# Optimization experiments

Hardware: AMD Instinct MI355X
Metric: run time of the kernel (lower is better)

Reference implementation:

```python
import jax, jax.numpy as jnp
import numpy as np

N_NODES = 100000
N_EDGES = 1600000
D_IN = 128
D_HID = 128
D_OUT = 16
N_LAYERS = 3
N_GRAPHS = 64
EPS = 1e-12


def _glorot(key, shape):
    fan_in = shape[-1]
    bound = 1.0 / np.sqrt(fan_in)
    return jax.random.uniform(key, shape, jnp.float32, -bound, bound)


def setup_inputs() -> dict:
    key = jax.random.key(0)
    ks = jax.random.split(key, 12)
    x = jax.random.normal(ks[0], (N_NODES, D_IN), jnp.float32)
    edge_index = jax.random.randint(ks[1], (2, N_EDGES), 0, N_NODES, jnp.int64)
    batch = jnp.sort(jax.random.randint(ks[2], (N_NODES,), 0, N_GRAPHS, jnp.int64))
    # stacked GraphSage weights: torch Linear stores [out, in]
    Wl = _glorot(ks[3], (N_LAYERS, D_HID, D_IN))
    bl = _glorot(ks[4], (N_LAYERS, D_HID))
    Wr = _glorot(ks[5], (N_LAYERS, D_HID, D_IN))
    br = _glorot(ks[6], (N_LAYERS, D_HID))
    W1 = _glorot(ks[7], (D_HID, D_HID))
    b1 = _glorot(ks[8], (D_HID,))
    W2 = _glorot(ks[9], (D_OUT, D_HID))
    b2 = _glorot(ks[10], (D_OUT,))
    return {"x": x, "edge_index": edge_index, "batch": batch,
            "Wl": Wl, "bl": bl, "Wr": Wr, "br": br,
            "W1": W1, "b1": b1, "W2": W2, "b2": b2}


def reference(x, edge_index, batch, Wl, bl, Wr, br, W1, b1, W2, b2):
    N = x.shape[0]
    src, dst = edge_index[0], edge_index[1]
    # in-degree for mean aggregation (clamped to avoid div-by-zero)
    deg = jax.ops.segment_sum(jnp.ones_like(dst, dtype=x.dtype), dst, num_segments=N)
    deg = jnp.maximum(deg, 1.0)[:, None]
    h = x
    for i in range(N_LAYERS):
        # lin_r applied at nodes, then gathered (equivalent to lin_r(x_j) per edge)
        hr = h @ Wr[i].T + br[i]
        msg = hr[src]                               # [E, D_HID] gather
        agg = jax.ops.segment_sum(msg, dst, num_segments=N) / deg  # scatter-mean
        out = agg + (h @ Wl[i].T + bl[i])
        # F.normalize(out) -> L2 norm along dim=1, eps=1e-12
        nrm = jnp.maximum(jnp.linalg.norm(out, axis=1, keepdims=True), EPS)
        h = jax.nn.relu(out / nrm)                  # dropout is identity (eval)
    # post message-passing MLP (dropout identity in eval mode)
    h = h @ W1.T + b1
    h = h @ W2.T + b2
    # global mean pool over graphs
    cnt = jnp.maximum(jax.ops.segment_sum(jnp.ones_like(batch, dtype=h.dtype), batch, num_segments=N_GRAPHS), 1.0)
    pooled = jax.ops.segment_sum(h, batch, num_segments=N_GRAPHS) / cnt[:, None]
    return jax.nn.log_softmax(pooled, axis=1)
```

## Files before the change

### kernel.cpp

```cpp
#include <hip/hip_runtime.h>
#include <cstdint>
#include <cstddef>

#define NN 100000
#define NE 1600000
#define DD 128
#define NG 64
#define NB 782
#define GB 1563

#if defined(__has_builtin)
#if __has_builtin(__builtin_amdgcn_cvt_pk_f32_fp8) && __has_builtin(__builtin_amdgcn_cvt_pk_fp8_f32)
#define USE_FP8 1
#endif
#endif
#ifndef USE_FP8
#define USE_FP8 0
#endif

using bf16x8 = __attribute__((ext_vector_type(8))) short;
using f32x4  = __attribute__((ext_vector_type(4))) float;
using f32x2  = __attribute__((ext_vector_type(2))) float;

__device__ __forceinline__ int clampi(int v, int hi) {
    v = v < 0 ? 0 : v;
    return v >= hi ? hi - 1 : v;
}
__device__ __forceinline__ unsigned short f2bf(float f) {
    unsigned int u = __float_as_uint(f);
    u += 0x7fffu + ((u >> 16) & 1u);
    return (unsigned short)(u >> 16);
}
__device__ __forceinline__ float bf2f(unsigned short s) {
    return __uint_as_float(((unsigned int)s) << 16);
}
#if USE_FP8
__device__ __forceinline__ unsigned char f2fp8(float v) {
    return (unsigned char)(__builtin_amdgcn_cvt_pk_fp8_f32(v, 0.f, 0, false) & 0xFF);
}
__device__ __forceinline__ void acc_row(f32x2* a2, uint2 v) {
    f32x2 p;
    p = __builtin_amdgcn_cvt_pk_f32_fp8(v.x, false); a2[0] += p;
    p = __builtin_amdgcn_cvt_pk_f32_fp8(v.x, true);  a2[1] += p;
    p = __builtin_amdgcn_cvt_pk_f32_fp8(v.y, false); a2[2] += p;
    p = __builtin_amdgcn_cvt_pk_f32_fp8(v.y, true);  a2[3] += p;
}
#endif

#define WTOT (3 * 256 * 128)
__global__ void cvtw_kernel(const float* __restrict__ Wl, const float* __restrict__ Wr,
                            unsigned short* __restrict__ Wcat3,
                            int* __restrict__ bcnt, int* __restrict__ gcur0,
                            float* __restrict__ pooled, float* __restrict__ cnt) {
    int t = blockIdx.x * 256 + threadIdx.x;
    if (t < NB) { bcnt[t] = 0; gcur0[t] = 0; }
    if (t < NG * DD) pooled[t] = 0.f;
    if (t < NG) cnt[t] = 0.f;
    if (t < WTOT) {
        int j    = t & 7;
        int lane = (t >> 3) & 63;
        int ks   = (t >> 9) & 3;
        int n    = (t >> 11) & 7;
        int half = (t >> 14) & 1;
        int l    = t >> 15;
        int l15 = lane & 15, lg = lane >> 4;
        int o = n * 16 + l15;
        int k = ks * 32 + lg * 8 + j;
        const float* Wsrc = half ? Wr : Wl;
        Wcat3[t] = f2bf(Wsrc[(size_t)l * 16384 + o * 128 + k]);
    }
}

template <bool F32IN>
__global__ __launch_bounds__(256) void gemm4_kernel(
    const void* __restrict__ hin_, const unsigned short* __restrict__ Wf,
    const float* __restrict__ bl, unsigned short* __restrict__ zb,
    unsigned char* __restrict__ ub, const int* __restrict__ dst,
    int* __restrict__ bcnt, int nG) {
    __shared__ unsigned short lA[64 * 128];
    __shared__ unsigned short sstz[64][136];

    if (blockIdx.x >= nG) {
        int* lcnt = (int*)lA;
        for (int i = threadIdx.x; i < NB; i += 256) lcnt[i] = 0;
        __syncthreads();
        int b = blockIdx.x - nG;
        int e0 = b * 8000;
        int e1 = e0 + 8000; if (e1 > NE) e1 = NE;
        for (int e = e0 + threadIdx.x; e < e1; e += 256)
            atomicAdd(&lcnt[clampi(dst[e], NN) >> 7], 1);
        __syncthreads();
        for (int i = threadIdx.x; i < NB; i += 256)
            if (lcnt[i]) atomicAdd(&bcnt[i], lcnt[i]);
        return;
    }

    const int tid = threadIdx.x;
    const int w = tid >> 6, l = tid & 63;
    const int l15 = l & 15, lg = l >> 4;
    const int n0 = blockIdx.x * 64;

#pragma unroll
    for (int q = 0; q < 4; ++q) {
        int d = (q * 256 + tid) * 16;
        int row = d >> 8;
        int colb = d & 255;
        int srow = n0 + row; srow = srow < NN ? srow : NN - 1;
        bf16x8 v;
        if (F32IN) {
            const float* rp = (const float*)hin_ + (size_t)srow * DD + (colb >> 1);
            const float4 f0 = *(const float4*)rp;
            const float4 f1 = *(const float4*)(rp + 4);
            v[0] = (short)f2bf(f0.x); v[1] = (short)f2bf(f0.y);
            v[2] = (short)f2bf(f0.z); v[3] = (short)f2bf(f0.w);
            v[4] = (short)f2bf(f1.x); v[5] = (short)f2bf(f1.y);
            v[6] = (short)f2bf(f1.z); v[7] = (short)f2bf(f1.w);
        } else {
            v = *(const bf16x8*)((const unsigned short*)hin_ + (size_t)srow * DD + (colb >> 1));
        }
        int sd = d ^ (((d >> 8) & 7) << 4);
        *(bf16x8*)((char*)lA + sd) = v;
    }
    __syncthreads();

    const int half = w >> 1, rt = w & 1;

    bf16x8 a[4][2];
#pragma unroll
    for (int ks = 0; ks < 4; ++ks)
#pragma unroll
        for (int m = 0; m < 2; ++m) {
            int row = rt * 32 + m * 16 + l15;
            int L = row * 256 + ks * 64 + lg * 16;
            int SL = L ^ (((L >> 8) & 7) << 4);
            a[ks][m] = *(const bf16x8*)((char*)lA + SL);
        }

    f32x4 acc[2][8];
#pragma unroll
    for (int m = 0; m < 2; ++m)
#pragma unroll
        for (int n = 0; n < 8; ++n) acc[m][n] = (f32x4){0.f, 0.f, 0.f, 0.f};

    const unsigned short* Wb = Wf + ((size_t)half << 14);
#pragma unroll
    for (int ks = 0; ks < 4; ++ks) {
#pragma unroll
        for (int n = 0; n < 8; ++n) {
            bf16x8 b = *(const bf16x8*)(Wb + (((n << 2) + ks) << 9) + (l << 3));
            acc[0][n] = __builtin_amdgcn_mfma_f32_16x16x32_bf16(a[ks][0], b, acc[0][n], 0, 0, 0);
            acc[1][n] = __builtin_amdgcn_mfma_f32_16x16x32_bf16(a[ks][1], b, acc[1][n], 0, 0, 0);
        }
    }

    __syncthreads();

    if (half == 0) {
        float blv[8];
#pragma unroll
        for (int n = 0; n < 8; ++n) blv[n] = bl[n * 16 + l15];
#pragma unroll
        for (int m = 0; m < 2; ++m)
#pragma unroll
            for (int r = 0; r < 4; ++r) {
                int brow = rt * 32 + m * 16 + lg * 4 + r;
#pragma unroll
                for (int n = 0; n < 8; ++n)
                    sstz[brow][n * 16 + l15] = f2bf(acc[m][n][r] + blv[n]);
            }
#pragma unroll
        for (int p = 0; p < 8; ++p) {
            int brow = rt * 32 + p * 4 + lg;
            int node = n0 + brow;
            bf16x8 vv = *(const bf16x8*)(&sstz[brow][l15 * 8]);
            if (node < NN)
                *(bf16x8*)(zb + (size_t)node * DD + l15 * 8) = vv;
        }
    } else {
#if USE_FP8
        unsigned char* sstu = (unsigned char*)lA;
#pragma unroll
        for (int m = 0; m < 2; ++m)
#pragma unroll
            for (int r = 0; r < 4; ++r) {
                int brow = rt * 32 + m * 16 + lg * 4 + r;
#pragma unroll
                for (int n = 0; n < 8; ++n)
                    sstu[brow * 136 + n * 16 + l15] = f2fp8(acc[m][n][r]);
            }
        __builtin_amdgcn_s_waitcnt(0);
#pragma unroll
        for (int p = 0; p < 8; ++p) {
            int brow = rt * 32 + p * 4 + lg;
            int node = n0 + brow;
            uint2 vv = *(const uint2*)(sstu + brow * 136 + l15 * 8);
            if (node < NN)
                *(uint2*)(ub + (size_t)node * DD + l15 * 8) = vv;
        }
#else
        unsigned short* ub16 = (unsigned short*)ub;
#pragma unroll
        for (int m = 0; m < 2; ++m)
#pragma unroll
            for (int r = 0; r < 4; ++r) {
                int brow = rt * 32 + m * 16 + lg * 4 + r;
                int node = n0 + brow;
                if (node < NN)
#pragma unroll
                    for (int n = 0; n < 8; ++n)
                        ub16[(size_t)node * DD + n * 16 + l15] = f2bf(acc[m][n][r]);
            }
#endif
    }
}

__global__ __launch_bounds__(256) void bpart2_kernel(
    const int* __restrict__ src, const int* __restrict__ dst,
    const int* __restrict__ bcnt, int* __restrict__ gcur0,
    int* __restrict__ bstart_g, unsigned* __restrict__ stage) {
    __shared__ int bst[NB];
    __shared__ int lcnt[NB];
    __shared__ int partial[256];
    const int t = threadIdx.x;
    int own[4]; int ssum = 0;
#pragma unroll
    for (int q = 0; q < 4; ++q) {
        int idx = t * 4 + q;
        own[q] = (idx < NB) ? bcnt[idx] : 0;
        ssum += own[q];
    }
    partial[t] = ssum;
    __syncthreads();
    for (int d = 1; d < 256; d <<= 1) {
        int v = (t >= d) ? partial[t - d] : 0;
        __syncthreads();
        partial[t] += v;
        __syncthreads();
    }
    int run = partial[t] - ssum;
#pragma unroll
    for (int q = 0; q < 4; ++q) {
        int idx = t * 4 + q;
        if (idx < NB) bst[idx] = run;
        run += own[q];
    }
    if (blockIdx.x == 0) {
#pragma unroll
        for (int q = 0; q < 4; ++q) {
            int idx = t * 4 + q;
            if (idx < NB) bstart_g[idx] = bst[idx];
        }
        if (t == 0) bstart_g[NB] = NE;
    }
    for (int i = t; i < NB; i += 256) lcnt[i] = 0;
    __syncthreads();
    int e0 = blockIdx.x * 8000;
    int e1 = e0 + 8000; if (e1 > NE) e1 = NE;
    for (int e = e0 + t; e < e1; e += 256)
        atomicAdd(&lcnt[clampi(dst[e], NN) >> 7], 1);
    __syncthreads();
    for (int i = t; i < NB; i += 256) {
        int c = lcnt[i];
        if (c) lcnt[i] = bst[i] + atomicAdd(&gcur0[i], c);
    }
    __syncthreads();
    for (int e = e0 + t; e < e1; e += 256) {
        int d = clampi(dst[e], NN);
        int pos = atomicAdd(&lcnt[d >> 7], 1);
        stage[pos] = (unsigned)clampi(src[e], NN) | ((unsigned)(d & 127) << 17);
    }
}

__global__ __launch_bounds__(256) void bfill_kernel(
    const unsigned* __restrict__ stage, const int* __restrict__ bstart,
    int* __restrict__ row_ptr, int* __restrict__ csr) {
    __shared__ int scnt[128];
    __shared__ int scur[128];
    const int b = blockIdx.x;
    const int t = threadIdx.x;
    const int s0 = bstart[b], s1 = bstart[b + 1];
    const int n0 = b << 7;
    int nend = NN - n0; if (nend > 128) nend = 128;
    if (t < 128) scnt[t] = 0;
    __syncthreads();
    for (int i = s0 + t; i < s1; i += 256)
        atomicAdd(&scnt[stage[i] >> 17], 1);
    __syncthreads();
    int own = (t < 128) ? scnt[t] : 0;
    for (int d = 1; d < 128; d <<= 1) {
        int v = (t < 128 && t >= d) ? scnt[t - d] : 0;
        __syncthreads();
        if (t < 128) scnt[t] += v;
        __syncthreads();
    }
    if (t < 128) {
        int excl = scnt[t] - own;
        scur[t] = excl;
        if (t < nend) row_ptr[n0 + t] = s0 + excl;
    }
    if (b == NB - 1 && t == 0) row_ptr[NN] = NE;
    __syncthreads();
    for (int i = s0 + t; i < s1; i += 256) {
        unsigned p = stage[i];
        int slot = atomicAdd(&scur[p >> 17], 1);
        csr[s0 + slot] = (int)(p & 0x1FFFFu);
    }
}

__global__ __launch_bounds__(256) void pullc4_kernel(
    const unsigned char* __restrict__ u, const unsigned short* __restrict__ z,
    const float* __restrict__ br, const int* __restrict__ row_ptr,
    const int* __restrict__ csr, unsigned short* __restrict__ hOut) {
    int w = threadIdx.x >> 6, lane = threadIdx.x & 63;
    int n = blockIdx.x * 4 + w;
    if (n >= NN) return;
    int g = lane >> 4, c = lane & 15;
    int s0 = row_ptr[n], s1 = row_ptr[n + 1];
    int len = s1 - s0;
    float inv = 1.0f / (float)(len > 0 ? len : 1);
    int idxv = (s0 + lane < s1) ? csr[s0 + lane] : 0;
    bf16x8 zv = *(const bf16x8*)(z + (size_t)n * DD + c * 8);
#if USE_FP8
    f32x2 a2[4];
#pragma unroll
    for (int q = 0; q < 4; ++q) a2[q] = (f32x2){0.f, 0.f};
    int lcap = len < 64 ? len : 64;
    int r = g;
    for (; r + 12 < lcap; r += 16) {
        int i0 = __shfl(idxv, r);
        int i1 = __shfl(idxv, r + 4);
        int i2 = __shfl(idxv, r + 8);
        int i3 = __shfl(idxv, r + 12);
        uint2 v0 = *(const uint2*)(u + (size_t)i0 * DD + c * 8);
        uint2 v1 = *(const uint2*)(u + (size_t)i1 * DD + c * 8);
        uint2 v2 = *(const uint2*)(u + (size_t)i2 * DD + c * 8);
        uint2 v3 = *(const uint2*)(u + (size_t)i3 * DD + c * 8);
        acc_row(a2, v0); acc_row(a2, v1); acc_row(a2, v2); acc_row(a2, v3);
    }
    for (; r < lcap; r += 4) {
        int i0 = __shfl(idxv, r);
        uint2 v0 = *(const uint2*)(u + (size_t)i0 * DD + c * 8);
        acc_row(a2, v0);
    }
    for (int j = s0 + 64 + g; j < s1; j += 4) {
        uint2 v0 = *(const uint2*)(u + (size_t)csr[j] * DD + c * 8);
        acc_row(a2, v0);
    }
    float acc[8];
#pragma unroll
    for (int q = 0; q < 4; ++q) { acc[q * 2] = a2[q].x; acc[q * 2 + 1] = a2[q].y; }
#else
    const unsigned short* ub16 = (const unsigned short*)u;
    float acc[8];
#pragma unroll
    for (int q = 0; q < 8; ++q) acc[q] = 0.f;
    int lcap = len < 64 ? len : 64;
    int r = g;
    for (; r < lcap; r += 4) {
        int i0 = __shfl(idxv, r);
        bf16x8 v0 = *(const bf16x8*)(ub16 + (size_t)i0 * DD + c * 8);
#pragma unroll
        for (int q = 0; q < 8; ++q) acc[q] += bf2f((unsigned short)v0[q]);
    }
    for (int j = s0 + 64 + g; j < s1; j += 4) {
        bf16x8 v0 = *(const bf16x8*)(ub16 + (size_t)csr[j] * DD + c * 8);
#pragma unroll
        for (int q = 0; q < 8; ++q) acc[q] += bf2f((unsigned short)v0[q]);
    }
#endif
#pragma unroll
    for (int q = 0; q < 8; ++q) {
        acc[q] += __shfl_xor(acc[q], 16);
        acc[q] += __shfl_xor(acc[q], 32);
    }
    const float4 br0 = *(const float4*)(br + c * 8);
    const float4 br1 = *(const float4*)(br + c * 8 + 4);
    float bg = len > 0 ? 1.f : 0.f;
    float v[8]; float ss = 0.f;
#pragma unroll
    for (int q = 0; q < 8; ++q) {
        float brq = (q < 4) ? (&br0.x)[q] : (&br1.x)[q - 4];
        v[q] = acc[q] * inv + bf2f((unsigned short)zv[q]) + bg * brq;
        ss = fmaf(v[q], v[q], ss);
    }
    ss += __shfl_xor(ss, 1); ss += __shfl_xor(ss, 2);
    ss += __shfl_xor(ss, 4); ss += __shfl_xor(ss, 8);
    float invn = 1.0f / fmaxf(sqrtf(ss), 1e-12f);
    if (g == 0) {
        bf16x8 rr;
#pragma unroll
        for (int q = 0; q < 8; ++q) rr[q] = (short)f2bf(fmaxf(v[q], 0.f) * invn);
        *(bf16x8*)(hOut + (size_t)n * DD + c * 8) = rr;
    }
}

__global__ __launch_bounds__(256) void pool_bf16(
    const unsigned short* __restrict__ h, const int* __restrict__ batch,
    float* __restrict__ pooled, float* __restrict__ cnt) {
    int hw = (blockIdx.x * blockDim.x + threadIdx.x) >> 5;
    int lane = threadIdx.x & 31;
    int total_hw = (gridDim.x * blockDim.x) >> 5;
    int chunk = (NN + total_hw - 1) / total_hw;
    int nbeg = hw * chunk;
    int nend = nbeg + chunk; if (nend > NN) nend = NN;
    if (nbeg >= nend) return;
    float ax = 0.f, ay = 0.f, az = 0.f, aw = 0.f;
    int curg = clampi(batch[nbeg], NG);
    int run = 0;
    for (int n = nbeg; n < nend; ++n) {
        int g = clampi(batch[n], NG);
        if (g != curg) {
            atomicAdd(&pooled[curg * DD + lane * 4 + 0], ax);
            atomicAdd(&pooled[curg * DD + lane * 4 + 1], ay);
            atomicAdd(&pooled[curg * DD + lane * 4 + 2], az);
            atomicAdd(&pooled[curg * DD + lane * 4 + 3], aw);
            if (lane == 0) atomicAdd(&cnt[curg], (float)run);
            ax = ay = az = aw = 0.f; run = 0; curg = g;
        }
        const ushort4 v = *(const ushort4*)(h + (size_t)n * DD + lane * 4);
        ax += bf2f(v.x); ay += bf2f(v.y); az += bf2f(v.z); aw += bf2f(v.w);
        ++run;
    }
    atomicAdd(&pooled[curg * DD + lane * 4 + 0], ax);
    atomicAdd(&pooled[curg * DD + lane * 4 + 1], ay);
    atomicAdd(&pooled[curg * DD + lane * 4 + 2], az);
    atomicAdd(&pooled[curg * DD + lane * 4 + 3], aw);
    if (lane == 0) atomicAdd(&cnt[curg], (float)run);
}

__global__ __launch_bounds__(1024) void tail_kernel(
    const float* __restrict__ pooled, const float* __restrict__ cnt,
    const float* __restrict__ W1, const float* __restrict__ b1,
    const float* __restrict__ W2, const float* __restrict__ b2,
    float* __restrict__ out) {
    __shared__ float Wc[16][128];
    __shared__ float bcs[16];
    int t = threadIdx.x;
    for (int i = t; i < 2048; i += 1024) {
        int o = i >> 7, k = i & 127;
        float s = 0.f;
        for (int j = 0; j < 128; ++j) s = fmaf(W2[o * 128 + j], W1[j * 128 + k], s);
        Wc[o][k] = s;
    }
    if (t < 16) {
        float sb = 0.f;
        for (int j = 0; j < 128; ++j) sb = fmaf(W2[t * 128 + j], b1[j], sb);
        bcs[t] = sb + b2[t];
    }
    __syncthreads();
    int g = t >> 4, o = t & 15;
    float invc = 1.0f / fmaxf(cnt[g], 1.0f);
    float z = bcs[o];
    for (int k = 0; k < 128; ++k) z = fmaf(pooled[g * DD + k] * invc, Wc[o][k], z);
    float m = z;
    m = fmaxf(m, __shfl_xor(m, 1)); m = fmaxf(m, __shfl_xor(m, 2));
    m = fmaxf(m, __shfl_xor(m, 4)); m = fmaxf(m, __shfl_xor(m, 8));
    float e = expf(z - m);
    float s = e;
    s += __shfl_xor(s, 1); s += __shfl_xor(s, 2);
    s += __shfl_xor(s, 4); s += __shfl_xor(s, 8);
    out[g * 16 + o] = z - m - logf(s);
}

__global__ void zero_out_kernel(float* __restrict__ out, int n) {
    int i = blockIdx.x * 256 + threadIdx.x;
    if (i < n) out[i] = 0.f;
}

extern "C" void kernel_launch(void* const* d_in, const int* in_sizes, int n_in,
                              void* d_out, int out_size, void* d_ws, size_t ws_size,
                              hipStream_t stream) {
    const float* x  = (const float*)d_in[0];
    const int*   ei = (const int*)d_in[1];
    const int* batch = (const int*)d_in[2];
    const float* Wl = (const float*)d_in[3];
    const float* bl = (const float*)d_in[4];
    const float* Wr = (const float*)d_in[5];
    const float* br = (const float*)d_in[6];
    const float* W1 = (const float*)d_in[7];
    const float* b1 = (const float*)d_in[8];
    const float* W2 = (const float*)d_in[9];
    const float* b2 = (const float*)d_in[10];
    float* out = (float*)d_out;

    const int* src = ei;
    const int* dst = ei + NE;

    char* ws = (char*)d_ws;
    size_t off = 0;
    auto alloc = [&](size_t bytes) -> void* {
        void* p = ws + off; off += (bytes + 255) & ~(size_t)255; return p;
    };
    unsigned short* hA    = (unsigned short*)alloc((size_t)NN * DD * 2);
    unsigned short* hB    = (unsigned short*)alloc((size_t)NN * DD * 2);
    unsigned short* zb    = (unsigned short*)alloc((size_t)NN * DD * 2);
    unsigned char*  ub    = (unsigned char*)alloc((size_t)NN * DD * 2);
    unsigned short* Wcat3 = (unsigned short*)alloc((size_t)WTOT * 2);
    int* row_ptr  = (int*)alloc((size_t)(NN + 1) * 4);
    int* csr      = (int*)alloc((size_t)NE * 4);
    unsigned* stage = (unsigned*)alloc((size_t)NE * 4);
    int* bcnt     = (int*)alloc((size_t)NB * 4);
    int* bstart   = (int*)alloc((size_t)(NB + 1) * 4);
    int* gcur0    = (int*)alloc((size_t)NB * 4);
    float* pooled = (float*)alloc(NG * DD * 4);
    float* cnt    = (float*)alloc(NG * 4);

    if (off > ws_size) {
        zero_out_kernel<<<(out_size + 255) / 256, 256, 0, stream>>>(out, out_size);
        return;
    }

    cvtw_kernel<<<(WTOT + 255) / 256, 256, 0, stream>>>(
        Wl, Wr, Wcat3, bcnt, gcur0, pooled, cnt);

    const int npb = (NE + 7999) / 8000;

    gemm4_kernel<true><<<GB + npb, 256, 0, stream>>>(
        x, Wcat3, bl, zb, ub, dst, bcnt, GB);

    bpart2_kernel<<<npb, 256, 0, stream>>>(src, dst, bcnt, gcur0, bstart, stage);
    bfill_kernel<<<NB, 256, 0, stream>>>(stage, bstart, row_ptr, csr);

    unsigned short* bufs[2] = {hA, hB};
    pullc4_kernel<<<(NN + 3) / 4, 256, 0, stream>>>(
        ub, zb, br, row_ptr, csr, bufs[0]);
    const unsigned short* hin = bufs[0];
    for (int l = 1; l < 3; ++l) {
        gemm4_kernel<false><<<GB, 256, 0, stream>>>(
            hin, Wcat3 + (size_t)l * 32768, bl + (size_t)l * 128,
            zb, ub, dst, bcnt, GB);
        pullc4_kernel<<<(NN + 3) / 4, 256, 0, stream>>>(
            ub, zb, br + (size_t)l * 128, row_ptr, csr, bufs[l & 1]);
        hin = bufs[l & 1];
    }

    pool_bf16<<<256, 256, 0, stream>>>(hin, batch, pooled, cnt);
    tail_kernel<<<1, 1024, 0, stream>>>(pooled, cnt, W1, b1, W2, b2, out);
}
```

Measured before the change: 350.1 us.

## Reshuffle CSR build stages and widen GEMM blocks to 512 threads

Moves the bucket-counting histogram into the weight-conversion kernel and folds the bucket partition (prefix scan plus staging scatter) into the first GEMM launch as extra blocks, so the separate bpart2 kernel disappears. The bcnt/gcur0 zeroing becomes a hipMemsetAsync over adjacent buffers. The GEMM switches to 512 threads with 8 waves, each computing a 16-row tile instead of 32, which halves per-wave accumulators and may raise occupancy. This removes one launch and overlaps partitioning with GEMM work, at the cost of a larger block and an extra memset call.

```diff
diff --git a/kernel.cpp b/kernel.cpp
--- a/kernel.cpp
+++ b/kernel.cpp
@@ -48,12 +48,27 @@
 #endif
 
 #define WTOT (3 * 256 * 128)
-__global__ void cvtw_kernel(const float* __restrict__ Wl, const float* __restrict__ Wr,
-                            unsigned short* __restrict__ Wcat3,
-                            int* __restrict__ bcnt, int* __restrict__ gcur0,
-                            float* __restrict__ pooled, float* __restrict__ cnt) {
+#define CVB 384
+__global__ __launch_bounds__(256) void cvth_kernel(
+    const float* __restrict__ Wl, const float* __restrict__ Wr,
+    unsigned short* __restrict__ Wcat3,
+    float* __restrict__ pooled, float* __restrict__ cnt,
+    const int* __restrict__ dst, int* __restrict__ bcnt) {
+    __shared__ int lcnt[NB];
+    if (blockIdx.x >= CVB) {
+        for (int i = threadIdx.x; i < NB; i += 256) lcnt[i] = 0;
+        __syncthreads();
+        int b = blockIdx.x - CVB;
+        int e0 = b * 8000;
+        int e1 = e0 + 8000; if (e1 > NE) e1 = NE;
+        for (int e = e0 + threadIdx.x; e < e1; e += 256)
+            atomicAdd(&lcnt[clampi(dst[e], NN) >> 7], 1);
+        __syncthreads();
+        for (int i = threadIdx.x; i < NB; i += 256)
+            if (lcnt[i]) atomicAdd(&bcnt[i], lcnt[i]);
+        return;
+    }
     int t = blockIdx.x * 256 + threadIdx.x;
-    if (t < NB) { bcnt[t] = 0; gcur0[t] = 0; }
     if (t < NG * DD) pooled[t] = 0.f;
     if (t < NG) cnt[t] = 0.f;
     if (t < WTOT) {
@@ -72,26 +87,69 @@
 }
 
 template <bool F32IN>
-__global__ __launch_bounds__(256) void gemm4_kernel(
+__global__ __launch_bounds__(512) void gemm5_kernel(
     const void* __restrict__ hin_, const unsigned short* __restrict__ Wf,
     const float* __restrict__ bl, unsigned short* __restrict__ zb,
-    unsigned char* __restrict__ ub, const int* __restrict__ dst,
-    int* __restrict__ bcnt, int nG) {
+    unsigned char* __restrict__ ub,
+    const int* __restrict__ src, const int* __restrict__ dst,
+    const int* __restrict__ bcnt, int* __restrict__ gcur0,
+    int* __restrict__ bstart_g, unsigned* __restrict__ stage, int nG) {
     __shared__ unsigned short lA[64 * 128];
     __shared__ unsigned short sstz[64][136];
 
     if (blockIdx.x >= nG) {
-        int* lcnt = (int*)lA;
-        for (int i = threadIdx.x; i < NB; i += 256) lcnt[i] = 0;
+        int* bst  = (int*)lA;
+        int* lcnt = (int*)(lA + 2048);
+        int* partial = (int*)(&sstz[0][0]);
+        const int t = threadIdx.x;
+        int own[2]; int ssum = 0;
+#pragma unroll
+        for (int q = 0; q < 2; ++q) {
+            int idx = t * 2 + q;
+            own[q] = (idx < NB) ? bcnt[idx] : 0;
+            ssum += own[q];
+        }
+        partial[t] = ssum;
+        __syncthreads();
+        for (int d = 1; d < 512; d <<= 1) {
+            int v = (t >= d) ? partial[t - d] : 0;
+            __syncthreads();
+            partial[t] += v;
+            __syncthreads();
+        }
+        int run = partial[t] - ssum;
+#pragma unroll
+        for (int q = 0; q < 2; ++q) {
+            int idx = t * 2 + q;
+            if (idx < NB) bst[idx] = run;
+            run += own[q];
+        }
+        if (blockIdx.x == nG) {
+#pragma unroll
+            for (int q = 0; q < 2; ++q) {
+                int idx = t * 2 + q;
+                if (idx < NB) bstart_g[idx] = bst[idx];
+            }
+            if (t == 0) bstart_g[NB] = NE;
+        }
+        for (int i = t; i < NB; i += 512) lcnt[i] = 0;
         __syncthreads();
         int b = blockIdx.x - nG;
         int e0 = b * 8000;
         int e1 = e0 + 8000; if (e1 > NE) e1 = NE;
-        for (int e = e0 + threadIdx.x; e < e1; e += 256)
+        for (int e = e0 + t; e < e1; e += 512)
             atomicAdd(&lcnt[clampi(dst[e], NN) >> 7], 1);
         __syncthreads();
-        for (int i = threadIdx.x; i < NB; i += 256)
-            if (lcnt[i]) atomicAdd(&bcnt[i], lcnt[i]);
+        for (int i = t; i < NB; i += 512) {
+            int c = lcnt[i];
+            if (c) lcnt[i] = bst[i] + atomicAdd(&gcur0[i], c);
+        }
+        __syncthreads();
+        for (int e = e0 + t; e < e1; e += 512) {
+            int d = clampi(dst[e], NN);
+            int pos = atomicAdd(&lcnt[d >> 7], 1);
+            stage[pos] = (unsigned)clampi(src[e], NN) | ((unsigned)(d & 127) << 17);
+        }
         return;
     }
 
@@ -101,8 +159,8 @@
     const int n0 = blockIdx.x * 64;
 
 #pragma unroll
-    for (int q = 0; q < 4; ++q) {
-        int d = (q * 256 + tid) * 16;
+    for (int q = 0; q < 2; ++q) {
+        int d = (q * 512 + tid) * 16;
         int row = d >> 8;
         int colb = d & 255;
         int srow = n0 + row; srow = srow < NN ? srow : NN - 1;
@@ -123,24 +181,20 @@
     }
     __syncthreads();
 
-    const int half = w >> 1, rt = w & 1;
-
-    bf16x8 a[4][2];
-#pragma unroll
-    for (int ks = 0; ks < 4; ++ks)
-#pragma unroll
-        for (int m = 0; m < 2; ++m) {
-            int row = rt * 32 + m * 16 + l15;
-            int L = row * 256 + ks * 64 + lg * 16;
-            int SL = L ^ (((L >> 8) & 7) << 4);
-            a[ks][m] = *(const bf16x8*)((char*)lA + SL);
-        }
-
-    f32x4 acc[2][8];
-#pragma unroll
-    for (int m = 0; m < 2; ++m)
-#pragma unroll
-        for (int n = 0; n < 8; ++n) acc[m][n] = (f32x4){0.f, 0.f, 0.f, 0.f};
+    const int half = w >> 2, rt = w & 3;
+
+    bf16x8 a[4];
+#pragma unroll
+    for (int ks = 0; ks < 4; ++ks) {
+        int row = rt * 16 + l15;
+        int L = row * 256 + ks * 64 + lg * 16;
+        int SL = L ^ (((L >> 8) & 7) << 4);
+        a[ks] = *(const bf16x8*)((char*)lA + SL);
+    }
+
+    f32x4 acc[8];
+#pragma unroll
+    for (int n = 0; n < 8; ++n) acc[n] = (f32x4){0.f, 0.f, 0.f, 0.f};
 
     const unsigned short* Wb = Wf + ((size_t)half << 14);
 #pragma unroll
@@ -148,8 +202,7 @@
 #pragma unroll
         for (int n = 0; n < 8; ++n) {
             bf16x8 b = *(const bf16x8*)(Wb + (((n << 2) + ks) << 9) + (l << 3));
-            acc[0][n] = __builtin_amdgcn_mfma_f32_16x16x32_bf16(a[ks][0], b, acc[0][n], 0, 0, 0);
-            acc[1][n] = __builtin_amdgcn_mfma_f32_16x16x32_bf16(a[ks][1], b, acc[1][n], 0, 0, 0);
+            acc[n] = __builtin_amdgcn_mfma_f32_16x16x32_bf16(a[ks], b, acc[n], 0, 0, 0);
         }
     }
 
@@ -160,17 +213,15 @@
 #pragma unroll
         for (int n = 0; n < 8; ++n) blv[n] = bl[n * 16 + l15];
 #pragma unroll
-        for (int m = 0; m < 2; ++m)
-#pragma unroll
-            for (int r = 0; r < 4; ++r) {
-                int brow = rt * 32 + m * 16 + lg * 4 + r;
-#pragma unroll
-                for (int n = 0; n < 8; ++n)
-                    sstz[brow][n * 16 + l15] = f2bf(acc[m][n][r] + blv[n]);
-            }
-#pragma unroll
-        for (int p = 0; p < 8; ++p) {
-            int brow = rt * 32 + p * 4 + lg;
+        for (int r = 0; r < 4; ++r) {
+            int brow = rt * 16 + lg * 4 + r;
+#pragma unroll
+            for (int n = 0; n < 8; ++n)
+                sstz[brow][n * 16 + l15] = f2bf(acc[n][r] + blv[n]);
+        }
+#pragma unroll
+        for (int p = 0; p < 4; ++p) {
+            int brow = rt * 16 + p * 4 + lg;
             int node = n0 + brow;
             bf16x8 vv = *(const bf16x8*)(&sstz[brow][l15 * 8]);
             if (node < NN)
@@ -180,18 +231,16 @@
 #if USE_FP8
         unsigned char* sstu = (unsigned char*)lA;
 #pragma unroll
-        for (int m = 0; m < 2; ++m)
-#pragma unroll
-            for (int r = 0; r < 4; ++r) {
-                int brow = rt * 32 + m * 16 + lg * 4 + r;
-#pragma unroll
-                for (int n = 0; n < 8; ++n)
-                    sstu[brow * 136 + n * 16 + l15] = f2fp8(acc[m][n][r]);
-            }
+        for (int r = 0; r < 4; ++r) {
+            int brow = rt * 16 + lg * 4 + r;
+#pragma unroll
+            for (int n = 0; n < 8; ++n)
+                sstu[brow * 136 + n * 16 + l15] = f2fp8(acc[n][r]);
+        }
         __builtin_amdgcn_s_waitcnt(0);
 #pragma unroll
-        for (int p = 0; p < 8; ++p) {
-            int brow = rt * 32 + p * 4 + lg;
+        for (int p = 0; p < 4; ++p) {
+            int brow = rt * 16 + p * 4 + lg;
             int node = n0 + brow;
             uint2 vv = *(const uint2*)(sstu + brow * 136 + l15 * 8);
             if (node < NN)
@@ -200,74 +249,15 @@
 #else
         unsigned short* ub16 = (unsigned short*)ub;
 #pragma unroll
-        for (int m = 0; m < 2; ++m)
-#pragma unroll
-            for (int r = 0; r < 4; ++r) {
-                int brow = rt * 32 + m * 16 + lg * 4 + r;
-                int node = n0 + brow;
-                if (node < NN)
-#pragma unroll
-                    for (int n = 0; n < 8; ++n)
-                        ub16[(size_t)node * DD + n * 16 + l15] = f2bf(acc[m][n][r]);
-            }
+        for (int r = 0; r < 4; ++r) {
+            int brow = rt * 16 + lg * 4 + r;
+            int node = n0 + brow;
+            if (node < NN)
+#pragma unroll
+                for (int n = 0; n < 8; ++n)
+                    ub16[(size_t)node * DD + n * 16 + l15] = f2bf(acc[n][r]);
+        }
 #endif
-    }
-}
-
-__global__ __launch_bounds__(256) void bpart2_kernel(
-    const int* __restrict__ src, const int* __restrict__ dst,
-    const int* __restrict__ bcnt, int* __restrict__ gcur0,
-    int* __restrict__ bstart_g, unsigned* __restrict__ stage) {
-    __shared__ int bst[NB];
-    __shared__ int lcnt[NB];
-    __shared__ int partial[256];
-    const int t = threadIdx.x;
-    int own[4]; int ssum = 0;
-#pragma unroll
-    for (int q = 0; q < 4; ++q) {
-        int idx = t * 4 + q;
-        own[q] = (idx < NB) ? bcnt[idx] : 0;
-        ssum += own[q];
-    }
-    partial[t] = ssum;
-    __syncthreads();
-    for (int d = 1; d < 256; d <<= 1) {
-        int v = (t >= d) ? partial[t - d] : 0;
-        __syncthreads();
-        partial[t] += v;
-        __syncthreads();
-    }
-    int run = partial[t] - ssum;
-#pragma unroll
-    for (int q = 0; q < 4; ++q) {
-        int idx = t * 4 + q;
-        if (idx < NB) bst[idx] = run;
-        run += own[q];
-    }
-    if (blockIdx.x == 0) {
-#pragma unroll
-        for (int q = 0; q < 4; ++q) {
-            int idx = t * 4 + q;
-            if (idx < NB) bstart_g[idx] = bst[idx];
-        }
-        if (t == 0) bstart_g[NB] = NE;
-    }
-    for (int i = t; i < NB; i += 256) lcnt[i] = 0;
-    __syncthreads();
-    int e0 = blockIdx.x * 8000;
-    int e1 = e0 + 8000; if (e1 > NE) e1 = NE;
-    for (int e = e0 + t; e < e1; e += 256)
-        atomicAdd(&lcnt[clampi(dst[e], NN) >> 7], 1);
-    __syncthreads();
-    for (int i = t; i < NB; i += 256) {
-        int c = lcnt[i];
-        if (c) lcnt[i] = bst[i] + atomicAdd(&gcur0[i], c);
-    }
-    __syncthreads();
-    for (int e = e0 + t; e < e1; e += 256) {
-        int d = clampi(dst[e], NN);
-        int pos = atomicAdd(&lcnt[d >> 7], 1);
-        stage[pos] = (unsigned)clampi(src[e], NN) | ((unsigned)(d & 127) << 17);
     }
 }
 
@@ -500,8 +490,8 @@
     int* csr      = (int*)alloc((size_t)NE * 4);
     unsigned* stage = (unsigned*)alloc((size_t)NE * 4);
     int* bcnt     = (int*)alloc((size_t)NB * 4);
+    int* gcur0    = (int*)alloc((size_t)NB * 4);
     int* bstart   = (int*)alloc((size_t)(NB + 1) * 4);
-    int* gcur0    = (int*)alloc((size_t)NB * 4);
     float* pooled = (float*)alloc(NG * DD * 4);
     float* cnt    = (float*)alloc(NG * 4);
 
@@ -510,15 +500,16 @@
         return;
     }
 
-    cvtw_kernel<<<(WTOT + 255) / 256, 256, 0, stream>>>(
-        Wl, Wr, Wcat3, bcnt, gcur0, pooled, cnt);
-
     const int npb = (NE + 7999) / 8000;
 
-    gemm4_kernel<true><<<GB + npb, 256, 0, stream>>>(
-        x, Wcat3, bl, zb, ub, dst, bcnt, GB);
-
-    bpart2_kernel<<<npb, 256, 0, stream>>>(src, dst, bcnt, gcur0, bstart, stage);
+    size_t bc_pad = ((size_t)NB * 4 + 255) & ~(size_t)255;
+    hipMemsetAsync(bcnt, 0, bc_pad * 2, stream);
+
+    cvth_kernel<<<CVB + npb, 256, 0, stream>>>(Wl, Wr, Wcat3, pooled, cnt, dst, bcnt);
+
+    gemm5_kernel<true><<<GB + npb, 512, 0, stream>>>(
+        x, Wcat3, bl, zb, ub, src, dst, bcnt, gcur0, bstart, stage, GB);
+
     bfill_kernel<<<NB, 256, 0, stream>>>(stage, bstart, row_ptr, csr);
 
     unsigned short* bufs[2] = {hA, hB};
@@ -526,9 +517,9 @@
         ub, zb, br, row_ptr, csr, bufs[0]);
     const unsigned short* hin = bufs[0];
     for (int l = 1; l < 3; ++l) {
-        gemm4_kernel<false><<<GB, 256, 0, stream>>>(
+        gemm5_kernel<false><<<GB, 512, 0, stream>>>(
             hin, Wcat3 + (size_t)l * 32768, bl + (size_t)l * 128,
-            zb, ub, dst, bcnt, GB);
+            zb, ub, src, dst, bcnt, gcur0, bstart, stage, GB);
         pullc4_kernel<<<(NN + 3) / 4, 256, 0, stream>>>(
             ub, zb, br + (size_t)l * 128, row_ptr, csr, bufs[l & 1]);
         hin = bufs[l & 1];
```

New measurement: 345.3 us (median of 2 runs). No clear change (-1.4%).

## Restage CSR build: count with weight convert, partition alongside first GEMM

Applied to the files above, without the earlier changes.

The per-bucket destination histogram moves out of the first GEMM launch and runs as extra blocks of the weight-conversion kernel. The bucket scan and stage partitioning, formerly a separate bpart2 kernel, now run as extra blocks of the first GEMM so they overlap with the matrix work. Counter zeroing is replaced by a hipMemsetAsync covering bcnt and gcur0, which are reordered so they sit next to each other in the workspace. This removes one kernel launch and its serial gap, at the cost of an extra memset call and larger shared-memory reuse inside the GEMM blocks.

```diff
diff --git a/kernel.cpp b/kernel.cpp
--- a/kernel.cpp
+++ b/kernel.cpp
@@ -48,12 +48,27 @@
 #endif
 
 #define WTOT (3 * 256 * 128)
-__global__ void cvtw_kernel(const float* __restrict__ Wl, const float* __restrict__ Wr,
-                            unsigned short* __restrict__ Wcat3,
-                            int* __restrict__ bcnt, int* __restrict__ gcur0,
-                            float* __restrict__ pooled, float* __restrict__ cnt) {
+#define CVB 384
+__global__ __launch_bounds__(256) void cvth_kernel(
+    const float* __restrict__ Wl, const float* __restrict__ Wr,
+    unsigned short* __restrict__ Wcat3,
+    float* __restrict__ pooled, float* __restrict__ cnt,
+    const int* __restrict__ dst, int* __restrict__ bcnt) {
+    __shared__ int lcnt[NB];
+    if (blockIdx.x >= CVB) {
+        for (int i = threadIdx.x; i < NB; i += 256) lcnt[i] = 0;
+        __syncthreads();
+        int b = blockIdx.x - CVB;
+        int e0 = b * 8000;
+        int e1 = e0 + 8000; if (e1 > NE) e1 = NE;
+        for (int e = e0 + threadIdx.x; e < e1; e += 256)
+            atomicAdd(&lcnt[clampi(dst[e], NN) >> 7], 1);
+        __syncthreads();
+        for (int i = threadIdx.x; i < NB; i += 256)
+            if (lcnt[i]) atomicAdd(&bcnt[i], lcnt[i]);
+        return;
+    }
     int t = blockIdx.x * 256 + threadIdx.x;
-    if (t < NB) { bcnt[t] = 0; gcur0[t] = 0; }
     if (t < NG * DD) pooled[t] = 0.f;
     if (t < NG) cnt[t] = 0.f;
     if (t < WTOT) {
@@ -72,26 +87,69 @@
 }
 
 template <bool F32IN>
-__global__ __launch_bounds__(256) void gemm4_kernel(
+__global__ __launch_bounds__(256) void gemm4b_kernel(
     const void* __restrict__ hin_, const unsigned short* __restrict__ Wf,
     const float* __restrict__ bl, unsigned short* __restrict__ zb,
-    unsigned char* __restrict__ ub, const int* __restrict__ dst,
-    int* __restrict__ bcnt, int nG) {
+    unsigned char* __restrict__ ub,
+    const int* __restrict__ src, const int* __restrict__ dst,
+    const int* __restrict__ bcnt, int* __restrict__ gcur0,
+    int* __restrict__ bstart_g, unsigned* __restrict__ stage, int nG) {
     __shared__ unsigned short lA[64 * 128];
     __shared__ unsigned short sstz[64][136];
 
     if (blockIdx.x >= nG) {
-        int* lcnt = (int*)lA;
-        for (int i = threadIdx.x; i < NB; i += 256) lcnt[i] = 0;
+        int* bst  = (int*)lA;
+        int* lcnt = (int*)(lA + 2048);
+        int* partial = (int*)(&sstz[0][0]);
+        const int t = threadIdx.x;
+        int own[4]; int ssum = 0;
+#pragma unroll
+        for (int q = 0; q < 4; ++q) {
+            int idx = t * 4 + q;
+            own[q] = (idx < NB) ? bcnt[idx] : 0;
+            ssum += own[q];
+        }
+        partial[t] = ssum;
+        __syncthreads();
+        for (int d = 1; d < 256; d <<= 1) {
+            int v = (t >= d) ? partial[t - d] : 0;
+            __syncthreads();
+            partial[t] += v;
+            __syncthreads();
+        }
+        int run = partial[t] - ssum;
+#pragma unroll
+        for (int q = 0; q < 4; ++q) {
+            int idx = t * 4 + q;
+            if (idx < NB) bst[idx] = run;
+            run += own[q];
+        }
+        if (blockIdx.x == nG) {
+#pragma unroll
+            for (int q = 0; q < 4; ++q) {
+                int idx = t * 4 + q;
+                if (idx < NB) bstart_g[idx] = bst[idx];
+            }
+            if (t == 0) bstart_g[NB] = NE;
+        }
+        for (int i = t; i < NB; i += 256) lcnt[i] = 0;
         __syncthreads();
         int b = blockIdx.x - nG;
         int e0 = b * 8000;
         int e1 = e0 + 8000; if (e1 > NE) e1 = NE;
-        for (int e = e0 + threadIdx.x; e < e1; e += 256)
+        for (int e = e0 + t; e < e1; e += 256)
             atomicAdd(&lcnt[clampi(dst[e], NN) >> 7], 1);
         __syncthreads();
-        for (int i = threadIdx.x; i < NB; i += 256)
-            if (lcnt[i]) atomicAdd(&bcnt[i], lcnt[i]);
+        for (int i = t; i < NB; i += 256) {
+            int c = lcnt[i];
+            if (c) lcnt[i] = bst[i] + atomicAdd(&gcur0[i], c);
+        }
+        __syncthreads();
+        for (int e = e0 + t; e < e1; e += 256) {
+            int d = clampi(dst[e], NN);
+            int pos = atomicAdd(&lcnt[d >> 7], 1);
+            stage[pos] = (unsigned)clampi(src[e], NN) | ((unsigned)(d & 127) << 17);
+        }
         return;
     }
 
@@ -211,63 +269,6 @@
                         ub16[(size_t)node * DD + n * 16 + l15] = f2bf(acc[m][n][r]);
             }
 #endif
-    }
-}
-
-__global__ __launch_bounds__(256) void bpart2_kernel(
-    const int* __restrict__ src, const int* __restrict__ dst,
-    const int* __restrict__ bcnt, int* __restrict__ gcur0,
-    int* __restrict__ bstart_g, unsigned* __restrict__ stage) {
-    __shared__ int bst[NB];
-    __shared__ int lcnt[NB];
-    __shared__ int partial[256];
-    const int t = threadIdx.x;
-    int own[4]; int ssum = 0;
-#pragma unroll
-    for (int q = 0; q < 4; ++q) {
-        int idx = t * 4 + q;
-        own[q] = (idx < NB) ? bcnt[idx] : 0;
-        ssum += own[q];
-    }
-    partial[t] = ssum;
-    __syncthreads();
-    for (int d = 1; d < 256; d <<= 1) {
-        int v = (t >= d) ? partial[t - d] : 0;
-        __syncthreads();
-        partial[t] += v;
-        __syncthreads();
-    }
-    int run = partial[t] - ssum;
-#pragma unroll
-    for (int q = 0; q < 4; ++q) {
-        int idx = t * 4 + q;
-        if (idx < NB) bst[idx] = run;
-        run += own[q];
-    }
-    if (blockIdx.x == 0) {
-#pragma unroll
-        for (int q = 0; q < 4; ++q) {
-            int idx = t * 4 + q;
-            if (idx < NB) bstart_g[idx] = bst[idx];
-        }
-        if (t == 0) bstart_g[NB] = NE;
-    }
-    for (int i = t; i < NB; i += 256) lcnt[i] = 0;
-    __syncthreads();
-    int e0 = blockIdx.x * 8000;
-    int e1 = e0 + 8000; if (e1 > NE) e1 = NE;
-    for (int e = e0 + t; e < e1; e += 256)
-        atomicAdd(&lcnt[clampi(dst[e], NN) >> 7], 1);
-    __syncthreads();
-    for (int i = t; i < NB; i += 256) {
-        int c = lcnt[i];
-        if (c) lcnt[i] = bst[i] + atomicAdd(&gcur0[i], c);
-    }
-    __syncthreads();
-    for (int e = e0 + t; e < e1; e += 256) {
-        int d = clampi(dst[e], NN);
-        int pos = atomicAdd(&lcnt[d >> 7], 1);
-        stage[pos] = (unsigned)clampi(src[e], NN) | ((unsigned)(d & 127) << 17);
     }
 }
 
@@ -500,8 +501,8 @@
     int* csr      = (int*)alloc((size_t)NE * 4);
     unsigned* stage = (unsigned*)alloc((size_t)NE * 4);
     int* bcnt     = (int*)alloc((size_t)NB * 4);
+    int* gcur0    = (int*)alloc((size_t)NB * 4);
     int* bstart   = (int*)alloc((size_t)(NB + 1) * 4);
-    int* gcur0    = (int*)alloc((size_t)NB * 4);
     float* pooled = (float*)alloc(NG * DD * 4);
     float* cnt    = (float*)alloc(NG * 4);
 
@@ -510,15 +511,16 @@
         return;
     }
 
-    cvtw_kernel<<<(WTOT + 255) / 256, 256, 0, stream>>>(
-        Wl, Wr, Wcat3, bcnt, gcur0, pooled, cnt);
-
     const int npb = (NE + 7999) / 8000;
 
-    gemm4_kernel<true><<<GB + npb, 256, 0, stream>>>(
-        x, Wcat3, bl, zb, ub, dst, bcnt, GB);
-
-    bpart2_kernel<<<npb, 256, 0, stream>>>(src, dst, bcnt, gcur0, bstart, stage);
+    size_t bc_pad = ((size_t)NB * 4 + 255) & ~(size_t)255;
+    hipMemsetAsync(bcnt, 0, bc_pad * 2, stream);
+
+    cvth_kernel<<<CVB + npb, 256, 0, stream>>>(Wl, Wr, Wcat3, pooled, cnt, dst, bcnt);
+
+    gemm4b_kernel<true><<<GB + npb, 256, 0, stream>>>(
+        x, Wcat3, bl, zb, ub, src, dst, bcnt, gcur0, bstart, stage, GB);
+
     bfill_kernel<<<NB, 256, 0, stream>>>(stage, bstart, row_ptr, csr);
 
     unsigned short* bufs[2] = {hA, hB};
@@ -526,9 +528,9 @@
         ub, zb, br, row_ptr, csr, bufs[0]);
     const unsigned short* hin = bufs[0];
     for (int l = 1; l < 3; ++l) {
-        gemm4_kernel<false><<<GB, 256, 0, stream>>>(
+        gemm4b_kernel<false><<<GB, 256, 0, stream>>>(
             hin, Wcat3 + (size_t)l * 32768, bl + (size_t)l * 128,
-            zb, ub, dst, bcnt, GB);
+            zb, ub, src, dst, bcnt, gcur0, bstart, stage, GB);
         pullc4_kernel<<<(NN + 3) / 4, 256, 0, stream>>>(
             ub, zb, br + (size_t)l * 128, row_ptr, csr, bufs[l & 1]);
         hin = bufs[l & 1];
```

Measured after the change: 348.9 us. About the same (-0.4%).
